# Kernel optimization log

Measured on AMD Instinct MI355X. Metric: run time of the kernel, lower is better.

## Reference

```python
import jax, jax.numpy as jnp
import numpy as np

D_NODE = 128
D_EDGE = 128
D_HID = 128
D_OUT = 128
N_NODES = 50000
N_EDGES = 500000
LN_EPS = 1e-5


def setup_inputs() -> dict:
    key = jax.random.key(0)
    ks = jax.random.split(key, 10)
    d_cat = 2 * D_NODE + D_EDGE  # 384
    inv = lambda d: 1.0 / np.sqrt(d)
    return {
        "efeat": jax.random.normal(ks[0], (N_EDGES, D_EDGE), jnp.float32),
        "nfeat": jax.random.normal(ks[1], (N_NODES, D_NODE), jnp.float32),
        "src": jax.random.randint(ks[2], (N_EDGES,), 0, N_NODES),
        "dst": jax.random.randint(ks[3], (N_EDGES,), 0, N_NODES),
        # MLP params: Linear(d_cat, hid) -> SiLU -> Linear(hid, out) -> LayerNorm(out)
        "W1": jax.random.uniform(ks[4], (d_cat, D_HID), jnp.float32, -inv(d_cat), inv(d_cat)),
        "b1": jnp.zeros((D_HID,), jnp.float32),
        "W2": jax.random.uniform(ks[5], (D_HID, D_OUT), jnp.float32, -inv(D_HID), inv(D_HID)),
        "b2": jnp.zeros((D_OUT,), jnp.float32),
        "gamma": jnp.ones((D_OUT,), jnp.float32),
        "beta": jnp.zeros((D_OUT,), jnp.float32),
    }


def _layernorm(x, gamma, beta):
    mu = jnp.mean(x, axis=-1, keepdims=True)
    var = jnp.mean(jnp.square(x - mu), axis=-1, keepdims=True)
    return (x - mu) * jax.lax.rsqrt(var + LN_EPS) * gamma + beta


def reference(efeat, nfeat, src, dst, W1, b1, W2, b2, gamma, beta):
    # gather source/target node feats per edge and concat with edge feats: [E, 2*Dn+De]
    cat_feat = jnp.concatenate([efeat, nfeat[src], nfeat[dst]], axis=-1)
    h = jax.nn.silu(cat_feat @ W1 + b1)          # [E, hid]
    out = _layernorm(h @ W2 + b2, gamma, beta)    # [E, out]
    efeat_new = out + efeat                        # residual
    return (efeat_new, nfeat)
```

## Files before the change

kernel.cpp:

```cpp
#include <hip/hip_runtime.h>
#include <hip/hip_bf16.h>

#define N_EDGES 500000
#define N_NODES 50000
#define NT ((N_EDGES + 63) / 64)
#define GRID 256
#define LN_EPS 1e-5f

typedef __attribute__((ext_vector_type(8))) short bf16x8;
typedef __attribute__((ext_vector_type(4))) short bf16x4;
typedef __attribute__((ext_vector_type(4))) float f32x4;

static __device__ __forceinline__ short f2bf(float f) {
  return __builtin_bit_cast(short, __float2bfloat16(f));
}
static __device__ __forceinline__ float bf2f(short s) {
  unsigned u = ((unsigned)(unsigned short)s) << 16;
  return __builtin_bit_cast(float, u);
}
static __device__ __forceinline__ void gload16(const void* g, void* l) {
  __builtin_amdgcn_global_load_lds(
      (const __attribute__((address_space(1))) unsigned int*)g,
      (__attribute__((address_space(3))) unsigned int*)l, 16, 0, 0);
}
static __device__ __forceinline__ void pin(bf16x8& v) {
  asm volatile("" : "+v"(v));
}
static __device__ __forceinline__ void bar_lds() {
  __builtin_amdgcn_sched_barrier(0);
  asm volatile("s_waitcnt lgkmcnt(0)" ::: "memory");
  __builtin_amdgcn_s_barrier();
  __builtin_amdgcn_sched_barrier(0);
}
static __device__ __forceinline__ void bar_vm8() {
  __builtin_amdgcn_sched_barrier(0);
  asm volatile("s_waitcnt vmcnt(8) lgkmcnt(0)" ::: "memory");
  __builtin_amdgcn_s_barrier();
  __builtin_amdgcn_sched_barrier(0);
}

__global__ void convert_kernel(const float* __restrict__ W1,
                               const float* __restrict__ W2,
                               const float* __restrict__ nfeat,
                               short* __restrict__ w1t, short* __restrict__ w2t,
                               short* __restrict__ nbf, float* __restrict__ outn) {
  const int step = gridDim.x * blockDim.x;
  const int t0 = blockIdx.x * blockDim.x + threadIdx.x;
  for (int i = t0; i < 384 * 128; i += step) {
    int n = i / 384, k = i - n * 384;
    w1t[i] = f2bf(W1[k * 128 + n]);
  }
  for (int i = t0; i < 128 * 128; i += step) {
    int n = i >> 7, k = i & 127;
    w2t[i] = f2bf(W2[k * 128 + n]);
  }
  for (int i = t0; i < N_NODES * 128 / 4; i += step) {
    f32x4 v = *(const f32x4*)(nfeat + (size_t)i * 4);
    short o4[4];
#pragma unroll
    for (int q = 0; q < 4; ++q) o4[q] = f2bf(v[q]);
    *(unsigned long long*)(nbf + (size_t)i * 4) = *(unsigned long long*)o4;
    *(f32x4*)(outn + (size_t)i * 4) = v;
  }
}

__global__ __launch_bounds__(512, 2) void edge_mlp_pipelined(
    const float* __restrict__ efeat, const short* __restrict__ nbf,
    const int* __restrict__ src, const int* __restrict__ dst,
    const short* __restrict__ w1t, const short* __restrict__ w2t,
    const float* __restrict__ b1, const float* __restrict__ b2,
    const float* __restrict__ gamma, const float* __restrict__ beta,
    float* __restrict__ out) {
  __shared__ __align__(16) char smem[132096];
  char* Hb = smem + 98304;
  char* xb = smem + 114688;
  float* gb = (float*)(smem + 131072);

  const int tid = threadIdx.x;
  const int lane = tid & 63;
  const int w = tid >> 6;
  const int wm = w >> 2;
  const int wn = w & 3;
  const int lrow = lane & 15;
  const int kgrp = (lane >> 4) & 3;
  if (tid < 256) gb[tid] = tid < 128 ? gamma[tid] : beta[tid - 128];

  bf16x8 B1r[12][2], B2r[4][2];
  float b1v[2], b2v[2];
#pragma unroll
  for (int n = 0; n < 2; ++n) {
    const int c = wn * 32 + n * 16 + lrow;
    b1v[n] = b1[c];
    b2v[n] = b2[c];
#pragma unroll
    for (int ks = 0; ks < 12; ++ks) {
      B1r[ks][n] = *(const bf16x8*)(w1t + c * 384 + ks * 32 + kgrp * 8);
      pin(B1r[ks][n]);
    }
#pragma unroll
    for (int ks = 0; ks < 4; ++ks) {
      B2r[ks][n] = *(const bf16x8*)(w2t + c * 128 + ks * 32 + kgrp * 8);
      pin(B2r[ks][n]);
    }
  }

  int grow[4], goff[4], gseg[4];
#pragma unroll
  for (int i = 0; i < 4; ++i) {
    int F = w * 4096 + i * 1024 + lane * 16;
    grow[i] = F >> 9;
    int win = F & 511;
    gseg[i] = win >> 8;
    goff[i] = (win & 255) ^ ((grow[i] & 15) << 4);
  }
  const int frow = tid >> 3;
  const int fcb = tid & 7;
  const int fswz = (frow & 15) << 4;

  f32x4 S[4];
  auto stage_S = [&](int t) {
    int e = t * 64 + frow;
    e = e < N_EDGES ? e : (N_EDGES - 1);
#pragma unroll
    for (int it = 0; it < 4; ++it)
      S[it] = *(const f32x4*)(efeat + (size_t)e * 128 + (fcb + it * 8) * 4);
  };
  auto write_ef = [&](char* buf) {
#pragma unroll
    for (int it = 0; it < 4; ++it) {
      bf16x4 v;
#pragma unroll
      for (int j = 0; j < 4; ++j) v[j] = f2bf(S[it][j]);
      *(bf16x4*)(buf + frow * 256 + (((fcb + it * 8) * 8) ^ fswz)) = v;
    }
  };
  int idxN[4];
  auto load_idx = [&](int t, int* ix) {
#pragma unroll
    for (int i = 0; i < 4; ++i) {
      int e = t * 64 + grow[i];
      e = e < N_EDGES ? e : (N_EDGES - 1);
      ix[i] = gseg[i] ? dst[e] : src[e];
    }
  };
  auto issue_g = [&](char* buf, const int* ix) {
#pragma unroll
    for (int i = 0; i < 4; ++i)
      gload16((const char*)nbf + (size_t)ix[i] * 256 + goff[i],
              buf + 16384 + w * 4096 + i * 1024);
  };

  const int t0 = blockIdx.x;
  char* cur = smem;
  char* nxt = smem + 49152;
  {
    int ix0[4];
    load_idx(t0, ix0);
    stage_S(t0);
    write_ef(cur);
    issue_g(cur, ix0);
    load_idx(t0 + GRID, idxN);
  }

  for (int t = t0; t < NT; t += GRID) {
    stage_S(t + GRID);
    issue_g(nxt, idxN);
    bar_vm8();
    load_idx(t + 2 * GRID, idxN);

    f32x4 acc[2][2];
#pragma unroll
    for (int m = 0; m < 2; ++m)
#pragma unroll
      for (int n = 0; n < 2; ++n) acc[m][n] = (f32x4)0.f;
#pragma unroll
    for (int ks = 0; ks < 12; ++ks) {
      bf16x8 a[2];
#pragma unroll
      for (int m = 0; m < 2; ++m) {
        int row = wm * 32 + m * 16 + lrow;
        int sw = (row & 15) << 4;
        a[m] = (ks < 4)
                   ? *(const bf16x8*)(cur + row * 256 + ((ks * 64 + kgrp * 16) ^ sw))
                   : *(const bf16x8*)(cur + 16384 + row * 512 +
                                      (((ks - 4) * 64 + kgrp * 16) ^ sw));
      }
#pragma unroll
      for (int m = 0; m < 2; ++m)
#pragma unroll
        for (int n = 0; n < 2; ++n)
          acc[m][n] = __builtin_amdgcn_mfma_f32_16x16x32_bf16(a[m], B1r[ks][n],
                                                              acc[m][n], 0, 0, 0);
    }

#pragma unroll
    for (int m = 0; m < 2; ++m)
#pragma unroll
      for (int n = 0; n < 2; ++n)
#pragma unroll
        for (int r = 0; r < 4; ++r) {
          float x = acc[m][n][r] + b1v[n];
          float h = x / (1.f + __expf(-x));
          int row = wm * 32 + m * 16 + kgrp * 4 + r;
          int col = wn * 32 + n * 16 + lrow;
          *(short*)(Hb + row * 256 + ((col * 2) ^ ((row & 15) << 4))) = f2bf(h);
        }
    bar_lds();

    f32x4 acc2[2][2];
#pragma unroll
    for (int m = 0; m < 2; ++m)
#pragma unroll
      for (int n = 0; n < 2; ++n) acc2[m][n] = (f32x4)0.f;
#pragma unroll
    for (int ks = 0; ks < 4; ++ks) {
      bf16x8 a[2];
#pragma unroll
      for (int m = 0; m < 2; ++m) {
        int row = wm * 32 + m * 16 + lrow;
        a[m] = *(const bf16x8*)(Hb + row * 256 +
                                ((ks * 64 + kgrp * 16) ^ ((row & 15) << 4)));
      }
#pragma unroll
      for (int m = 0; m < 2; ++m)
#pragma unroll
        for (int n = 0; n < 2; ++n)
          acc2[m][n] = __builtin_amdgcn_mfma_f32_16x16x32_bf16(a[m], B2r[ks][n],
                                                               acc2[m][n], 0, 0, 0);
    }

#pragma unroll
    for (int m = 0; m < 2; ++m)
#pragma unroll
      for (int n = 0; n < 2; ++n)
#pragma unroll
        for (int r = 0; r < 4; ++r) {
          float x = acc2[m][n][r] + b2v[n];
          int row = wm * 32 + m * 16 + kgrp * 4 + r;
          int col = wn * 32 + n * 16 + lrow;
          *(short*)(xb + row * 256 + ((col * 2) ^ ((row & 15) << 4))) = f2bf(x);
        }
    bar_lds();

    {
      bf16x4 xv[4];
      float s1 = 0.f, s2 = 0.f;
#pragma unroll
      for (int it = 0; it < 4; ++it) {
        int c4 = fcb + it * 8;
        xv[it] = *(const bf16x4*)(xb + frow * 256 + ((c4 * 8) ^ fswz));
#pragma unroll
        for (int j = 0; j < 4; ++j) {
          float f = bf2f(xv[it][j]);
          s1 += f;
          s2 += f * f;
        }
      }
      s1 += __shfl_xor(s1, 1, 64); s2 += __shfl_xor(s2, 1, 64);
      s1 += __shfl_xor(s1, 2, 64); s2 += __shfl_xor(s2, 2, 64);
      s1 += __shfl_xor(s1, 4, 64); s2 += __shfl_xor(s2, 4, 64);
      float mu = s1 * (1.f / 128.f);
      float var = s2 * (1.f / 128.f) - mu * mu;
      float rs = rsqrtf(var + LN_EPS);
      int e = t * 64 + frow;
      if (e < N_EDGES) {
        float* op = out + (size_t)e * 128;
#pragma unroll
        for (int it = 0; it < 4; ++it) {
          int c4 = fcb + it * 8;
          bf16x4 rv = *(const bf16x4*)(cur + frow * 256 + ((c4 * 8) ^ fswz));
          f32x4 g = *(const f32x4*)(gb + c4 * 4);
          f32x4 be = *(const f32x4*)(gb + 128 + c4 * 4);
          f32x4 o;
#pragma unroll
          for (int j = 0; j < 4; ++j)
            o[j] = (bf2f(xv[it][j]) - mu) * rs * g[j] + be[j] + bf2f(rv[j]);
          *(f32x4*)(op + c4 * 4) = o;
        }
      }
    }
    write_ef(nxt);
    char* tmp = cur; cur = nxt; nxt = tmp;
  }
  asm volatile("s_waitcnt vmcnt(0)" ::: "memory");
}

__global__ void edge_simple(const float* __restrict__ efeat, const float* __restrict__ nfeat,
                            const int* __restrict__ src, const int* __restrict__ dst,
                            const float* __restrict__ W1, const float* __restrict__ b1,
                            const float* __restrict__ W2, const float* __restrict__ b2,
                            const float* __restrict__ g, const float* __restrict__ be,
                            float* __restrict__ out) {
  int e = blockIdx.x, j = threadIdx.x;
  __shared__ float cat[384], h[128], red[128];
  cat[j] = efeat[(size_t)e * 128 + j];
  cat[128 + j] = nfeat[(size_t)src[e] * 128 + j];
  cat[256 + j] = nfeat[(size_t)dst[e] * 128 + j];
  __syncthreads();
  float s = b1[j];
  for (int k = 0; k < 384; ++k) s += cat[k] * W1[k * 128 + j];
  h[j] = s / (1.f + expf(-s));
  __syncthreads();
  float o = b2[j];
  for (int k = 0; k < 128; ++k) o += h[k] * W2[k * 128 + j];
  red[j] = o;
  __syncthreads();
  __shared__ float mu, rs;
  if (j == 0) {
    float s1 = 0, s2 = 0;
    for (int k = 0; k < 128; ++k) { s1 += red[k]; s2 += red[k] * red[k]; }
    mu = s1 / 128.f;
    rs = rsqrtf(s2 / 128.f - mu * mu + LN_EPS);
  }
  __syncthreads();
  out[(size_t)e * 128 + j] = (o - mu) * rs * g[j] + be[j] + efeat[(size_t)e * 128 + j];
}

extern "C" void kernel_launch(void* const* d_in, const int* in_sizes, int n_in,
                              void* d_out, int out_size, void* d_ws, size_t ws_size,
                              hipStream_t stream) {
  const float* efeat = (const float*)d_in[0];
  const float* nfeat = (const float*)d_in[1];
  const int* src = (const int*)d_in[2];
  const int* dst = (const int*)d_in[3];
  const float* W1 = (const float*)d_in[4];
  const float* b1 = (const float*)d_in[5];
  const float* W2 = (const float*)d_in[6];
  const float* b2 = (const float*)d_in[7];
  const float* gamma = (const float*)d_in[8];
  const float* beta = (const float*)d_in[9];
  float* out = (float*)d_out;

  short* w1t = (short*)d_ws;
  short* w2t = w1t + 384 * 128;
  short* nbf = w2t + 128 * 128;
  const size_t need =
      (size_t)(384 * 128 + 128 * 128 + (size_t)N_NODES * 128) * sizeof(short);

  if (ws_size >= need) {
    convert_kernel<<<1024, 256, 0, stream>>>(W1, W2, nfeat, w1t, w2t, nbf,
                                             out + (size_t)N_EDGES * 128);
    edge_mlp_pipelined<<<GRID, 512, 0, stream>>>(efeat, nbf, src, dst, w1t, w2t,
                                                 b1, b2, gamma, beta, out);
  } else {
    hipMemcpyAsync(out + (size_t)N_EDGES * 128, nfeat,
                   (size_t)N_NODES * 128 * sizeof(float),
                   hipMemcpyDeviceToDevice, stream);
    edge_simple<<<N_EDGES, 128, 0, stream>>>(efeat, nfeat, src, dst, W1, b1, W2,
                                             b2, gamma, beta, out);
  }
}
```

Baseline: 281.3 us.

## Double waves per block to 16, each owning a 16-column MFMA slice

```diff
diff --git a/kernel.cpp b/kernel.cpp
--- a/kernel.cpp
+++ b/kernel.cpp
@@ -32,9 +32,9 @@
   __builtin_amdgcn_s_barrier();
   __builtin_amdgcn_sched_barrier(0);
 }
-static __device__ __forceinline__ void bar_vm8() {
+static __device__ __forceinline__ void bar_vm4() {
   __builtin_amdgcn_sched_barrier(0);
-  asm volatile("s_waitcnt vmcnt(8) lgkmcnt(0)" ::: "memory");
+  asm volatile("s_waitcnt vmcnt(4) lgkmcnt(0)" ::: "memory");
   __builtin_amdgcn_s_barrier();
   __builtin_amdgcn_sched_barrier(0);
 }
@@ -64,7 +64,7 @@
   }
 }
 
-__global__ __launch_bounds__(512, 2) void edge_mlp_pipelined(
+__global__ __launch_bounds__(1024, 4) void edge_mlp_pipelined(
     const float* __restrict__ efeat, const short* __restrict__ nbf,
     const int* __restrict__ src, const int* __restrict__ dst,
     const short* __restrict__ w1t, const short* __restrict__ w2t,
@@ -79,65 +79,60 @@
   const int tid = threadIdx.x;
   const int lane = tid & 63;
   const int w = tid >> 6;
-  const int wm = w >> 2;
-  const int wn = w & 3;
+  const int wm = w >> 3;
+  const int wn = w & 7;
   const int lrow = lane & 15;
   const int kgrp = (lane >> 4) & 3;
   if (tid < 256) gb[tid] = tid < 128 ? gamma[tid] : beta[tid - 128];
 
-  bf16x8 B1r[12][2], B2r[4][2];
-  float b1v[2], b2v[2];
-#pragma unroll
-  for (int n = 0; n < 2; ++n) {
-    const int c = wn * 32 + n * 16 + lrow;
-    b1v[n] = b1[c];
-    b2v[n] = b2[c];
-#pragma unroll
-    for (int ks = 0; ks < 12; ++ks) {
-      B1r[ks][n] = *(const bf16x8*)(w1t + c * 384 + ks * 32 + kgrp * 8);
-      pin(B1r[ks][n]);
-    }
-#pragma unroll
-    for (int ks = 0; ks < 4; ++ks) {
-      B2r[ks][n] = *(const bf16x8*)(w2t + c * 128 + ks * 32 + kgrp * 8);
-      pin(B2r[ks][n]);
-    }
-  }
-
-  int grow[4], goff[4], gseg[4];
-#pragma unroll
-  for (int i = 0; i < 4; ++i) {
-    int F = w * 4096 + i * 1024 + lane * 16;
+  const int col = wn * 16 + lrow;
+  bf16x8 B1r[12], B2r[4];
+  const float b1v = b1[col], b2v = b2[col];
+#pragma unroll
+  for (int ks = 0; ks < 12; ++ks) {
+    B1r[ks] = *(const bf16x8*)(w1t + col * 384 + ks * 32 + kgrp * 8);
+    pin(B1r[ks]);
+  }
+#pragma unroll
+  for (int ks = 0; ks < 4; ++ks) {
+    B2r[ks] = *(const bf16x8*)(w2t + col * 128 + ks * 32 + kgrp * 8);
+    pin(B2r[ks]);
+  }
+
+  int grow[2], goff[2], gseg[2];
+#pragma unroll
+  for (int i = 0; i < 2; ++i) {
+    int F = w * 2048 + i * 1024 + lane * 16;
     grow[i] = F >> 9;
     int win = F & 511;
     gseg[i] = win >> 8;
     goff[i] = (win & 255) ^ ((grow[i] & 15) << 4);
   }
-  const int frow = tid >> 3;
-  const int fcb = tid & 7;
+  const int frow = tid >> 4;
+  const int fcb = tid & 15;
   const int fswz = (frow & 15) << 4;
 
-  f32x4 S[4];
+  f32x4 S[2];
   auto stage_S = [&](int t) {
     int e = t * 64 + frow;
     e = e < N_EDGES ? e : (N_EDGES - 1);
 #pragma unroll
-    for (int it = 0; it < 4; ++it)
-      S[it] = *(const f32x4*)(efeat + (size_t)e * 128 + (fcb + it * 8) * 4);
+    for (int it = 0; it < 2; ++it)
+      S[it] = *(const f32x4*)(efeat + (size_t)e * 128 + (fcb + it * 16) * 4);
   };
   auto write_ef = [&](char* buf) {
 #pragma unroll
-    for (int it = 0; it < 4; ++it) {
+    for (int it = 0; it < 2; ++it) {
       bf16x4 v;
 #pragma unroll
       for (int j = 0; j < 4; ++j) v[j] = f2bf(S[it][j]);
-      *(bf16x4*)(buf + frow * 256 + (((fcb + it * 8) * 8) ^ fswz)) = v;
+      *(bf16x4*)(buf + frow * 256 + (((fcb + it * 16) * 8) ^ fswz)) = v;
     }
   };
-  int idxN[4];
+  int idxN[2];
   auto load_idx = [&](int t, int* ix) {
 #pragma unroll
-    for (int i = 0; i < 4; ++i) {
+    for (int i = 0; i < 2; ++i) {
       int e = t * 64 + grow[i];
       e = e < N_EDGES ? e : (N_EDGES - 1);
       ix[i] = gseg[i] ? dst[e] : src[e];
@@ -145,16 +140,16 @@
   };
   auto issue_g = [&](char* buf, const int* ix) {
 #pragma unroll
-    for (int i = 0; i < 4; ++i)
+    for (int i = 0; i < 2; ++i)
       gload16((const char*)nbf + (size_t)ix[i] * 256 + goff[i],
-              buf + 16384 + w * 4096 + i * 1024);
+              buf + 16384 + w * 2048 + i * 1024);
   };
 
   const int t0 = blockIdx.x;
   char* cur = smem;
   char* nxt = smem + 49152;
   {
-    int ix0[4];
+    int ix0[2];
     load_idx(t0, ix0);
     stage_S(t0);
     write_ef(cur);
@@ -165,14 +160,12 @@
   for (int t = t0; t < NT; t += GRID) {
     stage_S(t + GRID);
     issue_g(nxt, idxN);
-    bar_vm8();
+    bar_vm4();
     load_idx(t + 2 * GRID, idxN);
 
-    f32x4 acc[2][2];
-#pragma unroll
-    for (int m = 0; m < 2; ++m)
-#pragma unroll
-      for (int n = 0; n < 2; ++n) acc[m][n] = (f32x4)0.f;
+    f32x4 acc[2];
+#pragma unroll
+    for (int m = 0; m < 2; ++m) acc[m] = (f32x4)0.f;
 #pragma unroll
     for (int ks = 0; ks < 12; ++ks) {
       bf16x8 a[2];
@@ -187,31 +180,23 @@
       }
 #pragma unroll
       for (int m = 0; m < 2; ++m)
-#pragma unroll
-        for (int n = 0; n < 2; ++n)
-          acc[m][n] = __builtin_amdgcn_mfma_f32_16x16x32_bf16(a[m], B1r[ks][n],
-                                                              acc[m][n], 0, 0, 0);
+        acc[m] = __builtin_amdgcn_mfma_f32_16x16x32_bf16(a[m], B1r[ks], acc[m], 0, 0, 0);
     }
 
 #pragma unroll
     for (int m = 0; m < 2; ++m)
 #pragma unroll
-      for (int n = 0; n < 2; ++n)
-#pragma unroll
-        for (int r = 0; r < 4; ++r) {
-          float x = acc[m][n][r] + b1v[n];
-          float h = x / (1.f + __expf(-x));
-          int row = wm * 32 + m * 16 + kgrp * 4 + r;
-          int col = wn * 32 + n * 16 + lrow;
-          *(short*)(Hb + row * 256 + ((col * 2) ^ ((row & 15) << 4))) = f2bf(h);
-        }
+      for (int r = 0; r < 4; ++r) {
+        float x = acc[m][r] + b1v;
+        float h = x / (1.f + __expf(-x));
+        int row = wm * 32 + m * 16 + kgrp * 4 + r;
+        *(short*)(Hb + row * 256 + ((col * 2) ^ ((row & 15) << 4))) = f2bf(h);
+      }
     bar_lds();
 
-    f32x4 acc2[2][2];
-#pragma unroll
-    for (int m = 0; m < 2; ++m)
-#pragma unroll
-      for (int n = 0; n < 2; ++n) acc2[m][n] = (f32x4)0.f;
+    f32x4 acc2[2];
+#pragma unroll
+    for (int m = 0; m < 2; ++m) acc2[m] = (f32x4)0.f;
 #pragma unroll
     for (int ks = 0; ks < 4; ++ks) {
       bf16x8 a[2];
@@ -223,31 +208,25 @@
       }
 #pragma unroll
       for (int m = 0; m < 2; ++m)
-#pragma unroll
-        for (int n = 0; n < 2; ++n)
-          acc2[m][n] = __builtin_amdgcn_mfma_f32_16x16x32_bf16(a[m], B2r[ks][n],
-                                                               acc2[m][n], 0, 0, 0);
+        acc2[m] = __builtin_amdgcn_mfma_f32_16x16x32_bf16(a[m], B2r[ks], acc2[m], 0, 0, 0);
     }
 
 #pragma unroll
     for (int m = 0; m < 2; ++m)
 #pragma unroll
-      for (int n = 0; n < 2; ++n)
-#pragma unroll
-        for (int r = 0; r < 4; ++r) {
-          float x = acc2[m][n][r] + b2v[n];
-          int row = wm * 32 + m * 16 + kgrp * 4 + r;
-          int col = wn * 32 + n * 16 + lrow;
-          *(short*)(xb + row * 256 + ((col * 2) ^ ((row & 15) << 4))) = f2bf(x);
-        }
+      for (int r = 0; r < 4; ++r) {
+        float x = acc2[m][r] + b2v;
+        int row = wm * 32 + m * 16 + kgrp * 4 + r;
+        *(short*)(xb + row * 256 + ((col * 2) ^ ((row & 15) << 4))) = f2bf(x);
+      }
     bar_lds();
 
     {
-      bf16x4 xv[4];
+      bf16x4 xv[2];
       float s1 = 0.f, s2 = 0.f;
 #pragma unroll
-      for (int it = 0; it < 4; ++it) {
-        int c4 = fcb + it * 8;
+      for (int it = 0; it < 2; ++it) {
+        int c4 = fcb + it * 16;
         xv[it] = *(const bf16x4*)(xb + frow * 256 + ((c4 * 8) ^ fswz));
 #pragma unroll
         for (int j = 0; j < 4; ++j) {
@@ -259,6 +238,7 @@
       s1 += __shfl_xor(s1, 1, 64); s2 += __shfl_xor(s2, 1, 64);
       s1 += __shfl_xor(s1, 2, 64); s2 += __shfl_xor(s2, 2, 64);
       s1 += __shfl_xor(s1, 4, 64); s2 += __shfl_xor(s2, 4, 64);
+      s1 += __shfl_xor(s1, 8, 64); s2 += __shfl_xor(s2, 8, 64);
       float mu = s1 * (1.f / 128.f);
       float var = s2 * (1.f / 128.f) - mu * mu;
       float rs = rsqrtf(var + LN_EPS);
@@ -266,8 +246,8 @@
       if (e < N_EDGES) {
         float* op = out + (size_t)e * 128;
 #pragma unroll
-        for (int it = 0; it < 4; ++it) {
-          int c4 = fcb + it * 8;
+        for (int it = 0; it < 2; ++it) {
+          int c4 = fcb + it * 16;
           bf16x4 rv = *(const bf16x4*)(cur + frow * 256 + ((c4 * 8) ^ fswz));
           f32x4 g = *(const f32x4*)(gb + c4 * 4);
           f32x4 be = *(const f32x4*)(gb + 128 + c4 * 4);
@@ -340,8 +320,8 @@
   if (ws_size >= need) {
     convert_kernel<<<1024, 256, 0, stream>>>(W1, W2, nfeat, w1t, w2t, nbf,
                                              out + (size_t)N_EDGES * 128);
-    edge_mlp_pipelined<<<GRID, 512, 0, stream>>>(efeat, nbf, src, dst, w1t, w2t,
-                                                 b1, b2, gamma, beta, out);
+    edge_mlp_pipelined<<<GRID, 1024, 0, stream>>>(efeat, nbf, src, dst, w1t, w2t,
+                                                  b1, b2, gamma, beta, out);
   } else {
     hipMemcpyAsync(out + (size_t)N_EDGES * 128, nfeat,
                    (size_t)N_NODES * 128 * sizeof(float),
```

New measurement: 395.8 us. +40.7%, slower.
